# Kernel tuning notes

Hardware: AMD Instinct MI355X
Metric: run time of the kernel (lower is better)

## Reference

```python
import jax, jax.numpy as jnp
import numpy as np

B, H, S, D = 4, 16, 2048, 64


def setup_inputs() -> dict:
    key = jax.random.key(0)
    kq, kk, kv, kp = jax.random.split(key, 4)
    query = jax.random.normal(kq, (B, H, S, D), dtype=jnp.float32)
    k = jax.random.normal(kk, (B, H, S, D), dtype=jnp.float32)
    value = jax.random.normal(kv, (B, H, S, D), dtype=jnp.float32)
    # 0/1 key-padding mask, broadcastable against the [S, S] causal mask
    padding_mask = jax.random.randint(kp, (B, 1, 1, S), 0, 2, dtype=jnp.int32)
    return {"query": query, "key": k, "value": value, "padding_mask": padding_mask}


def reference(query, key, value, padding_mask):
    d_k = query.shape[-1]
    seq_len = query.shape[-2]
    # scores: [B, H, S, S]
    scores = jnp.einsum("bhqd,bhkd->bhqk", query, key) / jnp.sqrt(jnp.float32(d_k))
    # causal mask: 1 above diagonal
    future = jnp.triu(jnp.ones((seq_len, seq_len), dtype=jnp.float32), k=1)
    combined = future + padding_mask.astype(jnp.float32)  # values in {0,1,2}
    # faithful to torch masked_fill(combined_mask == 1, -1e9): only exact 1 is masked
    scores = jnp.where(combined == 1.0, jnp.float32(-1e9), scores)
    attention_weights = jax.nn.softmax(scores, axis=-1)
    result = attention_weights @ value  # [B, H, S, D]
    return result, attention_weights
```

## Files before the change

### kernel.cpp

```cpp
#include <hip/hip_runtime.h>

#define SEQ 2048
#define DH  64
#define NH  16
#define NB  4
#define NHEADS (NB * NH)
#define NKT 32
#define QT  64
#define NQT (SEQ / QT)
#define NBLK (NHEADS * NQT)
#define KTILE_SH 8192
#define QTILE_SH 8192

typedef _Float16 f16x8 __attribute__((ext_vector_type(8)));
typedef _Float16 f16x4 __attribute__((ext_vector_type(4)));
typedef short    s16x8 __attribute__((ext_vector_type(8)));
typedef float    f32x4 __attribute__((ext_vector_type(4)));

#define MF32(a,b,c) __builtin_amdgcn_mfma_f32_16x16x32_f16(a,b,c,0,0,0)
#define MF16(a,b,c) __builtin_amdgcn_mfma_f32_16x16x16f16(a,b,c,0,0,0)

static __device__ __forceinline__ short f16b(float x) {
    _Float16 h = (_Float16)x;
    return __builtin_bit_cast(short, h);
}

__global__ __launch_bounds__(256) void prep(
    const float* __restrict__ Q, const float* __restrict__ K,
    const float* __restrict__ V, const int* __restrict__ pad,
    short* __restrict__ qimg, short* __restrict__ kimg,
    short* __restrict__ vimg, unsigned* __restrict__ pm)
{
    const int t    = threadIdx.x;
    const int kt   = blockIdx.x & (NKT - 1);
    const int head = blockIdx.x >> 5;
    const size_t rowbase = ((size_t)head * SEQ + (size_t)kt * 64) * DH;

    {
        const int row = t >> 2;
        const int c0  = (t & 3) * 16;
        const int lj  = row & 15;

        {
            const float4* gp = (const float4*)(K + rowbase + (size_t)row * DH + c0);
            const float4 v0 = gp[0], v1 = gp[1], v2 = gp[2], v3 = gp[3];
            const float x[16] = {v0.x,v0.y,v0.z,v0.w, v1.x,v1.y,v1.z,v1.w,
                                 v2.x,v2.y,v2.z,v2.w, v3.x,v3.y,v3.z,v3.w};
            short* tb = kimg + ((size_t)head * NKT + kt) * KTILE_SH + (row >> 4) * 2048;
#pragma unroll
            for (int cg = 0; cg < 2; ++cg) {
                const int col0 = c0 + cg * 8;
                const int dh = col0 >> 5, lg = (col0 & 31) >> 3;
                s16x8 hi8, lo8;
#pragma unroll
                for (int j = 0; j < 8; ++j) {
                    const float xv = x[cg * 8 + j];
                    _Float16 h = (_Float16)xv;
                    hi8[j] = __builtin_bit_cast(short, h);
                    lo8[j] = f16b(xv - (float)h);
                }
                *(s16x8*)&tb[dh * 1024 +       (lg * 16 + lj) * 8] = hi8;
                *(s16x8*)&tb[dh * 1024 + 512 + (lg * 16 + lj) * 8] = lo8;
            }
        }
        {
            const float4* gp = (const float4*)(Q + rowbase + (size_t)row * DH + c0);
            const float4 v0 = gp[0], v1 = gp[1], v2 = gp[2], v3 = gp[3];
            const float x[16] = {v0.x,v0.y,v0.z,v0.w, v1.x,v1.y,v1.z,v1.w,
                                 v2.x,v2.y,v2.z,v2.w, v3.x,v3.y,v3.z,v3.w};
            const int m = row >> 4;
            short* tb = qimg + ((size_t)head * NQT + kt) * QTILE_SH + m * 2048;
#pragma unroll
            for (int cg = 0; cg < 2; ++cg) {
                const int col0 = c0 + cg * 8;
                const int dh = col0 >> 5, lg = (col0 & 31) >> 3;
                s16x8 hi8, lo8;
#pragma unroll
                for (int j = 0; j < 8; ++j) {
                    const float xv = x[cg * 8 + j];
                    _Float16 h = (_Float16)xv;
                    hi8[j] = __builtin_bit_cast(short, h);
                    lo8[j] = f16b(xv - (float)h);
                }
                *(s16x8*)&tb[dh * 1024 +       (lg * 16 + lj) * 8] = hi8;
                *(s16x8*)&tb[dh * 1024 + 512 + (lg * 16 + lj) * 8] = lo8;
            }
        }
    }
    {
        const int kc = t >> 6, l = t & 63;
        const int lg = l >> 4, lj = l & 15;
        short* tb = vimg + ((size_t)head * NKT + kt) * KTILE_SH + kc * 2048;
#pragma unroll
        for (int dt = 0; dt < 4; ++dt) {
            s16x8 o;
#pragma unroll
            for (int j = 0; j < 4; ++j) {
                const float xv = V[rowbase + (size_t)(kc * 16 + lg * 4 + j) * DH + dt * 16 + lj];
                _Float16 h = (_Float16)xv;
                o[j]     = __builtin_bit_cast(short, h);
                o[4 + j] = f16b(xv - (float)h);
            }
            *(s16x8*)&tb[dt * 512 + l * 8] = o;
        }
    }
    if (blockIdx.x == 0) {
        const int b = t >> 6, klc = t & 63;
        unsigned mword = 0;
#pragma unroll
        for (int kt2 = 0; kt2 < NKT; ++kt2)
            mword |= (unsigned)(pad[b * SEQ + kt2 * 64 + klc] & 1) << kt2;
        pm[t] = mword;
    }
}

struct KF { f16x8 h0, l0, h1, l1; };
struct VF { f16x8 v0, v1, v2, v3; };

#define LDKF(dst_, kt_) do {                                                   \
    const short* p_ = kb + (size_t)(kt_) * KTILE_SH;                           \
    dst_.h0 = *(const f16x8*)(p_ +        l * 8);                              \
    dst_.l0 = *(const f16x8*)(p_ +  512 + l * 8);                              \
    dst_.h1 = *(const f16x8*)(p_ + 1024 + l * 8);                              \
    dst_.l1 = *(const f16x8*)(p_ + 1536 + l * 8);                              \
} while (0)

#define LDVF(dst_, kt_) do {                                                   \
    const short* p_ = vb + (size_t)(kt_) * KTILE_SH;                           \
    dst_.v0 = *(const f16x8*)(p_ +        l * 8);                              \
    dst_.v1 = *(const f16x8*)(p_ +  512 + l * 8);                              \
    dst_.v2 = *(const f16x8*)(p_ + 1024 + l * 8);                              \
    dst_.v3 = *(const f16x8*)(p_ + 1536 + l * 8);                              \
} while (0)

#define QK24(kf_, a0_, a1_, a2_, a3_) do {                                     \
    a0_ = MF32(kf_.h0, qh[0][0], a0_);  a1_ = MF32(kf_.h0, qh[1][0], a1_);     \
    a2_ = MF32(kf_.h0, qh[2][0], a2_);  a3_ = MF32(kf_.h0, qh[3][0], a3_);     \
    a0_ = MF32(kf_.h0, ql[0][0], a0_);  a1_ = MF32(kf_.h0, ql[1][0], a1_);     \
    a2_ = MF32(kf_.h0, ql[2][0], a2_);  a3_ = MF32(kf_.h0, ql[3][0], a3_);     \
    a0_ = MF32(kf_.l0, qh[0][0], a0_);  a1_ = MF32(kf_.l0, qh[1][0], a1_);     \
    a2_ = MF32(kf_.l0, qh[2][0], a2_);  a3_ = MF32(kf_.l0, qh[3][0], a3_);     \
    a0_ = MF32(kf_.h1, qh[0][1], a0_);  a1_ = MF32(kf_.h1, qh[1][1], a1_);     \
    a2_ = MF32(kf_.h1, qh[2][1], a2_);  a3_ = MF32(kf_.h1, qh[3][1], a3_);     \
    a0_ = MF32(kf_.h1, ql[0][1], a0_);  a1_ = MF32(kf_.h1, ql[1][1], a1_);     \
    a2_ = MF32(kf_.h1, ql[2][1], a2_);  a3_ = MF32(kf_.h1, ql[3][1], a3_);     \
    a0_ = MF32(kf_.l1, qh[0][1], a0_);  a1_ = MF32(kf_.l1, qh[1][1], a1_);     \
    a2_ = MF32(kf_.l1, qh[2][1], a2_);  a3_ = MF32(kf_.l1, qh[3][1], a3_);     \
} while (0)

#define P1BODY(kt_, kf_, vf_) do {                                             \
    f32x4 a0_ = (f32x4){0.f,0.f,0.f,0.f}, a1_ = (f32x4){0.f,0.f,0.f,0.f};      \
    f32x4 a2_ = (f32x4){0.f,0.f,0.f,0.f}, a3_ = (f32x4){0.f,0.f,0.f,0.f};      \
    QK24(kf_, a0_, a1_, a2_, a3_);                                             \
    const int kab_ = (kt_) * 64 + wk * 16 + lg * 4;                            \
    f16x4 w16_[4];                                                             \
    _Pragma("unroll") for (int m = 0; m < 4; ++m) {                            \
        const f32x4 av_ = (m==0) ? a0_ : (m==1) ? a1_ : (m==2) ? a2_ : a3_;    \
        const int qg_ = qglob + m * 16;                                        \
        float e_[4];                                                           \
        _Pragma("unroll") for (int r = 0; r < 4; ++r) {                        \
            const int ka_ = kab_ + r;                                          \
            const int pd_ = (int)((pmq[r] >> (kt_)) & 1u);                     \
            const bool msk_ = ((ka_ > qg_) != (pd_ == 1));                     \
            e_[r] = __expf((msk_ ? -8.0e9f : av_[r]) * 0.125f);                \
        }                                                                      \
        rs[m] += (e_[0] + e_[1]) + (e_[2] + e_[3]);                            \
        w16_[m] = (f16x4){(_Float16)e_[0], (_Float16)e_[1],                    \
                          (_Float16)e_[2], (_Float16)e_[3]};                   \
    }                                                                          \
    _Pragma("unroll") for (int dt = 0; dt < 4; ++dt) {                         \
        const f16x8 vv_ = (dt==0) ? vf_.v0 : (dt==1) ? vf_.v1                  \
                        : (dt==2) ? vf_.v2 : vf_.v3;                           \
        const f16x4 vh_ = __builtin_shufflevector(vv_, vv_, 0,1,2,3);          \
        const f16x4 vl_ = __builtin_shufflevector(vv_, vv_, 4,5,6,7);          \
        ov[0][dt] = MF16(w16_[0], vh_, ov[0][dt]);                             \
        ov[1][dt] = MF16(w16_[1], vh_, ov[1][dt]);                             \
        ov[2][dt] = MF16(w16_[2], vh_, ov[2][dt]);                             \
        ov[3][dt] = MF16(w16_[3], vh_, ov[3][dt]);                             \
        ov[0][dt] = MF16(w16_[0], vl_, ov[0][dt]);                             \
        ov[1][dt] = MF16(w16_[1], vl_, ov[1][dt]);                             \
        ov[2][dt] = MF16(w16_[2], vl_, ov[2][dt]);                             \
        ov[3][dt] = MF16(w16_[3], vl_, ov[3][dt]);                             \
    }                                                                          \
} while (0)

#define P2BODY(kt_, kf_) do {                                                  \
    f32x4 a0_ = (f32x4){0.f,0.f,0.f,0.f}, a1_ = (f32x4){0.f,0.f,0.f,0.f};      \
    f32x4 a2_ = (f32x4){0.f,0.f,0.f,0.f}, a3_ = (f32x4){0.f,0.f,0.f,0.f};      \
    QK24(kf_, a0_, a1_, a2_, a3_);                                             \
    const int kab_ = (kt_) * 64 + wk * 16 + lg * 4;                            \
    _Pragma("unroll") for (int m = 0; m < 4; ++m) {                            \
        const f32x4 av_ = (m==0) ? a0_ : (m==1) ? a1_ : (m==2) ? a2_ : a3_;    \
        const int qg_ = qglob + m * 16;                                        \
        float e_[4];                                                           \
        _Pragma("unroll") for (int r = 0; r < 4; ++r) {                        \
            const int ka_ = kab_ + r;                                          \
            const int pd_ = (int)((pmq[r] >> (kt_)) & 1u);                     \
            const bool msk_ = ((ka_ > qg_) != (pd_ == 1));                     \
            e_[r] = __expf((msk_ ? -8.0e9f : av_[r]) * 0.125f);                \
        }                                                                      \
        f32x4 w4_;                                                             \
        w4_[0] = e_[0] * invr[m]; w4_[1] = e_[1] * invr[m];                    \
        w4_[2] = e_[2] * invr[m]; w4_[3] = e_[3] * invr[m];                    \
        __builtin_nontemporal_store(w4_, (f32x4*)&out_w[wbm[m] + kab_]);       \
    }                                                                          \
} while (0)

__global__ __launch_bounds__(256, 2) void attn_fwd(
    const short* __restrict__ QI, const short* __restrict__ KI,
    const short* __restrict__ VI, const unsigned* __restrict__ PM,
    float* __restrict__ out_res, float* __restrict__ out_w)
{
    __shared__ float s_op[4][QT][65];
    __shared__ float s_red[QT][4];

    const int t = threadIdx.x;
    int bid = blockIdx.x;
    bid = (bid & 7) * (NBLK / 8) + (bid >> 3);

    const int qtile = bid & (NQT - 1);
    const int head  = bid >> 5;
    const int q0    = qtile * QT;
    const size_t hoff = (size_t)head * SEQ * DH;
    const size_t woff = (size_t)head * SEQ * SEQ;

    const int l  = t & 63;
    const int wk = t >> 6;
    const int lj = l & 15;
    const int lg = l >> 4;
    const int qglob = q0 + lj;

    const short* kb  = KI + (size_t)head * NKT * KTILE_SH + wk * 2048;
    const short* vb  = VI + (size_t)head * NKT * KTILE_SH + wk * 2048;
    const short* qbp = QI + ((size_t)head * NQT + qtile) * QTILE_SH;

    f16x8 qh[4][2], ql[4][2];
#pragma unroll
    for (int m = 0; m < 4; ++m)
#pragma unroll
        for (int dh = 0; dh < 2; ++dh) {
            qh[m][dh] = *(const f16x8*)(qbp + m * 2048 + dh * 1024 +       l * 8);
            ql[m][dh] = *(const f16x8*)(qbp + m * 2048 + dh * 1024 + 512 + l * 8);
        }

    int pmq[4];
#pragma unroll
    for (int r = 0; r < 4; ++r)
        pmq[r] = PM[(head >> 4) * 64 + wk * 16 + lg * 4 + r];

    float rs[4] = {0.f, 0.f, 0.f, 0.f};
    f32x4 ov[4][4];
#pragma unroll
    for (int m = 0; m < 4; ++m)
#pragma unroll
        for (int dt = 0; dt < 4; ++dt) ov[m][dt] = (f32x4){0.f,0.f,0.f,0.f};

    KF kfA, kfB;
    VF vfA, vfB;
    LDKF(kfA, 0);
    LDVF(vfA, 0);
#pragma unroll 1
    for (int it = 0; it < NKT / 2; ++it) {
        const int kt0 = it * 2, kt1 = kt0 + 1;
        LDKF(kfB, kt1);
        LDVF(vfB, kt1);
        P1BODY(kt0, kfA, vfA);
        LDKF(kfA, (kt1 + 1) & (NKT - 1));
        LDVF(vfA, (kt1 + 1) & (NKT - 1));
        P1BODY(kt1, kfB, vfB);
    }

#pragma unroll
    for (int m = 0; m < 4; ++m) {
        float v = rs[m];
        v += __shfl_xor(v, 16, 64);
        v += __shfl_xor(v, 32, 64);
        rs[m] = v;
    }
    if (lg == 0) {
#pragma unroll
        for (int m = 0; m < 4; ++m)
            s_red[m * 16 + lj][wk] = rs[m];
    }
#pragma unroll
    for (int m = 0; m < 4; ++m)
#pragma unroll
        for (int dt = 0; dt < 4; ++dt)
#pragma unroll
            for (int r = 0; r < 4; ++r)
                s_op[wk][m * 16 + lg * 4 + r][dt * 16 + lj] = ov[m][dt][r];
    __syncthreads();

    {
        const int q  = t >> 2;
        const int c0 = (t & 3) * 16;
        const float inv = 1.0f / (s_red[q][0] + s_red[q][1] + s_red[q][2] + s_red[q][3]);
        float* op = out_res + hoff + (size_t)(q0 + q) * DH + c0;
#pragma unroll
        for (int g = 0; g < 4; ++g) {
            float4 o;
            o.x = (s_op[0][q][c0+g*4+0]+s_op[1][q][c0+g*4+0]+s_op[2][q][c0+g*4+0]+s_op[3][q][c0+g*4+0]) * inv;
            o.y = (s_op[0][q][c0+g*4+1]+s_op[1][q][c0+g*4+1]+s_op[2][q][c0+g*4+1]+s_op[3][q][c0+g*4+1]) * inv;
            o.z = (s_op[0][q][c0+g*4+2]+s_op[1][q][c0+g*4+2]+s_op[2][q][c0+g*4+2]+s_op[3][q][c0+g*4+2]) * inv;
            o.w = (s_op[0][q][c0+g*4+3]+s_op[1][q][c0+g*4+3]+s_op[2][q][c0+g*4+3]+s_op[3][q][c0+g*4+3]) * inv;
            *(float4*)(op + g * 4) = o;
        }
    }

    float invr[4];
    size_t wbm[4];
#pragma unroll
    for (int m = 0; m < 4; ++m) {
        const int qq = m * 16 + lj;
        invr[m] = 1.0f / (s_red[qq][0] + s_red[qq][1] + s_red[qq][2] + s_red[qq][3]);
        wbm[m]  = woff + (size_t)(q0 + qq) * SEQ;
    }

    LDKF(kfA, 0);
#pragma unroll 1
    for (int it = 0; it < NKT / 2; ++it) {
        const int kt0 = it * 2, kt1 = kt0 + 1;
        LDKF(kfB, kt1);
        P2BODY(kt0, kfA);
        LDKF(kfA, (kt1 + 1) & (NKT - 1));
        P2BODY(kt1, kfB);
    }
}

extern "C" void kernel_launch(void* const* d_in, const int* in_sizes, int n_in,
                              void* d_out, int out_size, void* d_ws, size_t ws_size,
                              hipStream_t stream) {
    const float* Q   = (const float*)d_in[0];
    const float* K   = (const float*)d_in[1];
    const float* V   = (const float*)d_in[2];
    const int*   pad = (const int*)d_in[3];
    float* out_res = (float*)d_out;
    float* out_w   = out_res + (size_t)NB * NH * SEQ * DH;

    short* qimg = (short*)d_ws;
    short* kimg = qimg + (size_t)NHEADS * NQT * QTILE_SH;
    short* vimg = kimg + (size_t)NHEADS * NKT * KTILE_SH;
    unsigned* pm = (unsigned*)(vimg + (size_t)NHEADS * NKT * KTILE_SH);

    prep<<<dim3(NHEADS * NKT), 256, 0, stream>>>(Q, K, V, pad, qimg, kimg, vimg, pm);
    attn_fwd<<<dim3(NBLK), 256, 0, stream>>>(qimg, kimg, vimg, pm, out_res, out_w);
}
```

Measured before the change: 1.280 ms.

## Split Q to fp16 hi/lo inside attention kernel and use plain weight stores

```diff
diff --git a/kernel.cpp b/kernel.cpp
--- a/kernel.cpp
+++ b/kernel.cpp
@@ -10,7 +10,6 @@
 #define NQT (SEQ / QT)
 #define NBLK (NHEADS * NQT)
 #define KTILE_SH 8192
-#define QTILE_SH 8192
 
 typedef _Float16 f16x8 __attribute__((ext_vector_type(8)));
 typedef _Float16 f16x4 __attribute__((ext_vector_type(4)));
@@ -26,10 +25,9 @@
 }
 
 __global__ __launch_bounds__(256) void prep(
-    const float* __restrict__ Q, const float* __restrict__ K,
-    const float* __restrict__ V, const int* __restrict__ pad,
-    short* __restrict__ qimg, short* __restrict__ kimg,
-    short* __restrict__ vimg, unsigned* __restrict__ pm)
+    const float* __restrict__ K, const float* __restrict__ V,
+    const int* __restrict__ pad,
+    short* __restrict__ kimg, short* __restrict__ vimg, unsigned* __restrict__ pm)
 {
     const int t    = threadIdx.x;
     const int kt   = blockIdx.x & (NKT - 1);
@@ -40,51 +38,25 @@
         const int row = t >> 2;
         const int c0  = (t & 3) * 16;
         const int lj  = row & 15;
-
-        {
-            const float4* gp = (const float4*)(K + rowbase + (size_t)row * DH + c0);
-            const float4 v0 = gp[0], v1 = gp[1], v2 = gp[2], v3 = gp[3];
-            const float x[16] = {v0.x,v0.y,v0.z,v0.w, v1.x,v1.y,v1.z,v1.w,
-                                 v2.x,v2.y,v2.z,v2.w, v3.x,v3.y,v3.z,v3.w};
-            short* tb = kimg + ((size_t)head * NKT + kt) * KTILE_SH + (row >> 4) * 2048;
-#pragma unroll
-            for (int cg = 0; cg < 2; ++cg) {
-                const int col0 = c0 + cg * 8;
-                const int dh = col0 >> 5, lg = (col0 & 31) >> 3;
-                s16x8 hi8, lo8;
-#pragma unroll
-                for (int j = 0; j < 8; ++j) {
-                    const float xv = x[cg * 8 + j];
-                    _Float16 h = (_Float16)xv;
-                    hi8[j] = __builtin_bit_cast(short, h);
-                    lo8[j] = f16b(xv - (float)h);
-                }
-                *(s16x8*)&tb[dh * 1024 +       (lg * 16 + lj) * 8] = hi8;
-                *(s16x8*)&tb[dh * 1024 + 512 + (lg * 16 + lj) * 8] = lo8;
+        const float4* gp = (const float4*)(K + rowbase + (size_t)row * DH + c0);
+        const float4 v0 = gp[0], v1 = gp[1], v2 = gp[2], v3 = gp[3];
+        const float x[16] = {v0.x,v0.y,v0.z,v0.w, v1.x,v1.y,v1.z,v1.w,
+                             v2.x,v2.y,v2.z,v2.w, v3.x,v3.y,v3.z,v3.w};
+        short* tb = kimg + ((size_t)head * NKT + kt) * KTILE_SH + (row >> 4) * 2048;
+#pragma unroll
+        for (int cg = 0; cg < 2; ++cg) {
+            const int col0 = c0 + cg * 8;
+            const int dh = col0 >> 5, lg = (col0 & 31) >> 3;
+            s16x8 hi8, lo8;
+#pragma unroll
+            for (int j = 0; j < 8; ++j) {
+                const float xv = x[cg * 8 + j];
+                _Float16 h = (_Float16)xv;
+                hi8[j] = __builtin_bit_cast(short, h);
+                lo8[j] = f16b(xv - (float)h);
             }
-        }
-        {
-            const float4* gp = (const float4*)(Q + rowbase + (size_t)row * DH + c0);
-            const float4 v0 = gp[0], v1 = gp[1], v2 = gp[2], v3 = gp[3];
-            const float x[16] = {v0.x,v0.y,v0.z,v0.w, v1.x,v1.y,v1.z,v1.w,
-                                 v2.x,v2.y,v2.z,v2.w, v3.x,v3.y,v3.z,v3.w};
-            const int m = row >> 4;
-            short* tb = qimg + ((size_t)head * NQT + kt) * QTILE_SH + m * 2048;
-#pragma unroll
-            for (int cg = 0; cg < 2; ++cg) {
-                const int col0 = c0 + cg * 8;
-                const int dh = col0 >> 5, lg = (col0 & 31) >> 3;
-                s16x8 hi8, lo8;
-#pragma unroll
-                for (int j = 0; j < 8; ++j) {
-                    const float xv = x[cg * 8 + j];
-                    _Float16 h = (_Float16)xv;
-                    hi8[j] = __builtin_bit_cast(short, h);
-                    lo8[j] = f16b(xv - (float)h);
-                }
-                *(s16x8*)&tb[dh * 1024 +       (lg * 16 + lj) * 8] = hi8;
-                *(s16x8*)&tb[dh * 1024 + 512 + (lg * 16 + lj) * 8] = lo8;
-            }
+            *(s16x8*)&tb[dh * 1024 +       (lg * 16 + lj) * 8] = hi8;
+            *(s16x8*)&tb[dh * 1024 + 512 + (lg * 16 + lj) * 8] = lo8;
         }
     }
     {
@@ -202,12 +174,12 @@
         f32x4 w4_;                                                             \
         w4_[0] = e_[0] * invr[m]; w4_[1] = e_[1] * invr[m];                    \
         w4_[2] = e_[2] * invr[m]; w4_[3] = e_[3] * invr[m];                    \
-        __builtin_nontemporal_store(w4_, (f32x4*)&out_w[wbm[m] + kab_]);       \
+        *(f32x4*)&out_w[wbm[m] + kab_] = w4_;      \
     }                                                                          \
 } while (0)
 
 __global__ __launch_bounds__(256, 2) void attn_fwd(
-    const short* __restrict__ QI, const short* __restrict__ KI,
+    const float* __restrict__ Qf, const short* __restrict__ KI,
     const short* __restrict__ VI, const unsigned* __restrict__ PM,
     float* __restrict__ out_res, float* __restrict__ out_w)
 {
@@ -230,17 +202,27 @@
     const int lg = l >> 4;
     const int qglob = q0 + lj;
 
-    const short* kb  = KI + (size_t)head * NKT * KTILE_SH + wk * 2048;
-    const short* vb  = VI + (size_t)head * NKT * KTILE_SH + wk * 2048;
-    const short* qbp = QI + ((size_t)head * NQT + qtile) * QTILE_SH;
+    const short* kb = KI + (size_t)head * NKT * KTILE_SH + wk * 2048;
+    const short* vb = VI + (size_t)head * NKT * KTILE_SH + wk * 2048;
 
     f16x8 qh[4][2], ql[4][2];
 #pragma unroll
     for (int m = 0; m < 4; ++m)
 #pragma unroll
         for (int dh = 0; dh < 2; ++dh) {
-            qh[m][dh] = *(const f16x8*)(qbp + m * 2048 + dh * 1024 +       l * 8);
-            ql[m][dh] = *(const f16x8*)(qbp + m * 2048 + dh * 1024 + 512 + l * 8);
+            const float* qp = Qf + hoff + (size_t)(q0 + m * 16 + lj) * DH + dh * 32 + lg * 8;
+            const float4 a = *(const float4*)qp;
+            const float4 b = *(const float4*)(qp + 4);
+            const float x[8] = {a.x,a.y,a.z,a.w, b.x,b.y,b.z,b.w};
+            f16x8 hv, lv;
+#pragma unroll
+            for (int j = 0; j < 8; ++j) {
+                _Float16 h = (_Float16)x[j];
+                hv[j] = h;
+                lv[j] = (_Float16)(x[j] - (float)h);
+            }
+            qh[m][dh] = hv;
+            ql[m][dh] = lv;
         }
 
     int pmq[4];
@@ -337,11 +319,10 @@
     float* out_res = (float*)d_out;
     float* out_w   = out_res + (size_t)NB * NH * SEQ * DH;
 
-    short* qimg = (short*)d_ws;
-    short* kimg = qimg + (size_t)NHEADS * NQT * QTILE_SH;
+    short* kimg = (short*)d_ws;
     short* vimg = kimg + (size_t)NHEADS * NKT * KTILE_SH;
     unsigned* pm = (unsigned*)(vimg + (size_t)NHEADS * NKT * KTILE_SH);
 
-    prep<<<dim3(NHEADS * NKT), 256, 0, stream>>>(Q, K, V, pad, qimg, kimg, vimg, pm);
-    attn_fwd<<<dim3(NBLK), 256, 0, stream>>>(qimg, kimg, vimg, pm, out_res, out_w);
+    prep<<<dim3(NHEADS * NKT), 256, 0, stream>>>(K, V, pad, kimg, vimg, pm);
+    attn_fwd<<<dim3(NBLK), 256, 0, stream>>>(Q, kimg, vimg, pm, out_res, out_w);
 }
```

Result: slower. 1.453 ms (+13.5%).
